# Performance work log

Hardware: AMD Instinct MI355X
Metric: run time of the kernel (lower is better)

The kernel has to match this reference:

```python
import jax, jax.numpy as jnp
import numpy as np

N, F, E, LIN, C, B = 16384, 500, 128, 128, 10, 4096
P_EDGE = 0.002  # ~32 avg degree


def _l2norm(x):
    # F.normalize(dim=1), eps=1e-12
    n = jnp.linalg.norm(x, axis=1, keepdims=True)
    return x / jnp.maximum(n, 1e-12)


def setup_inputs() -> dict:
    key = jax.random.key(0)
    ks = jax.random.split(key, 10)
    adj = (jax.random.uniform(ks[0], (N, N)) < P_EDGE).astype(jnp.float32)
    idx = jnp.arange(N)
    adj = adj.at[idx, idx].set(1.0)  # self-loops guarantee degree >= 1
    data = jax.random.normal(ks[1], (N, F), dtype=jnp.float32)
    nodes = jax.random.randint(ks[2], (B,), 0, N)
    # Encoder 1: Linear(2F -> E); Encoder 2: Linear(2E -> E); classifier heads
    W1 = jax.random.normal(ks[3], (E, 2 * F), dtype=jnp.float32) * 0.03
    b1 = jnp.zeros((E,), jnp.float32)
    W2 = jax.random.normal(ks[4], (E, 2 * E), dtype=jnp.float32) * 0.06
    b2 = jnp.zeros((E,), jnp.float32)
    Wl1 = jax.random.normal(ks[5], (LIN, E), dtype=jnp.float32) * 0.08
    bl1 = jnp.zeros((LIN,), jnp.float32)
    Wl2 = jax.random.normal(ks[6], (C, LIN), dtype=jnp.float32) * 0.12
    bl2 = jnp.zeros((C,), jnp.float32)
    return {"nodes": nodes, "adj": adj, "data": data,
            "W1": W1, "b1": b1, "W2": W2, "b2": b2,
            "Wl1": Wl1, "bl1": bl1, "Wl2": Wl2, "bl2": bl2}


def reference(nodes, adj, data, W1, b1, W2, b2, Wl1, bl1, Wl2, bl2):
    deg = jnp.sum(adj, axis=1, keepdims=True)  # [N,1]
    # Layer 1 (mean aggregator over full neighbor set): computed for all nodes
    neigh1 = (adj @ data) / deg                               # [N,F]
    h1 = jnp.concatenate([data, neigh1], axis=1)              # [N,2F] (self, neigh)
    H1 = _l2norm(jax.nn.relu(h1 @ W1.T + b1))                 # [N,E]
    # Layer 2: only for the queried node batch
    neigh2 = (adj[nodes] @ H1) / deg[nodes]                   # [B,E]
    h2 = jnp.concatenate([H1[nodes], neigh2], axis=1)         # [B,2E]
    H2 = _l2norm(jax.nn.relu(h2 @ W2.T + b2))                 # [B,E]
    x = H2 @ Wl1.T + bl1                                      # [B,LIN]
    x = x @ Wl2.T + bl2                                       # [B,C]
    return jax.nn.softmax(x, axis=1)
```

## Files before the change

### kernel.cpp

```cpp
#include <hip/hip_runtime.h>
#include <math.h>
#include <stddef.h>

#define N_NODES 16384
#define F_DIM   500
#define E_DIM   128
#define C_DIM   10
#define B_DIM   4096
#define MAXDEG  128

typedef __attribute__((ext_vector_type(8))) short short8;
typedef __attribute__((ext_vector_type(4))) float f32x4;

__device__ inline unsigned short f2bf(float f) {
    union { float f; unsigned int u; } v; v.f = f;
    unsigned int u = v.u;
    u += 0x7FFFu + ((u >> 16) & 1u);
    return (unsigned short)(u >> 16);
}
__device__ inline float bf2f(unsigned short u) {
    union { unsigned int u; float f; } v; v.u = (unsigned int)u << 16;
    return v.f;
}
__device__ inline short8 cvt8(float4 a, float4 b) {
    short8 v;
    v[0] = (short)f2bf(a.x); v[1] = (short)f2bf(a.y);
    v[2] = (short)f2bf(a.z); v[3] = (short)f2bf(a.w);
    v[4] = (short)f2bf(b.x); v[5] = (short)f2bf(b.y);
    v[6] = (short)f2bf(b.z); v[7] = (short)f2bf(b.w);
    return v;
}

__global__ __launch_bounds__(256) void k_fuse1(const float* __restrict__ data,
                                               const float* __restrict__ W1,
                                               const float* __restrict__ W2,
                                               const float* __restrict__ Wl1,
                                               const float* __restrict__ adj,
                                               unsigned short* __restrict__ Xb16,
                                               unsigned short* __restrict__ nbr,
                                               int* __restrict__ deg,
                                               unsigned short* __restrict__ W2ab16,
                                               unsigned short* __restrict__ W2bb16,
                                               float* __restrict__ Wl1t) {
    __shared__ alignas(16) unsigned char smem[4352];
    const int bb = blockIdx.x;
    const int tid = threadIdx.x;

    if (bb < 64) {
        int idx = bb * 256 + tid;
        int n = idx >> 7, k = idx & 127;
        W2ab16[idx] = f2bf(W2[(size_t)n * 256 + k]);
        return;
    } else if (bb < 128) {
        int idx = (bb - 64) * 256 + tid;
        int n = idx >> 7, k = idx & 127;
        W2bb16[idx] = f2bf(W2[(size_t)n * 256 + 128 + k]);
        return;
    } else if (bb < 144) {
        float (*tile)[33] = (float (*)[33])smem;
        int tb = bb - 128;
        int k0 = (tb & 3) * 32, e0 = (tb >> 2) * 32;
        int tx = tid & 31, ty0 = tid >> 5;
#pragma unroll
        for (int q = 0; q < 4; ++q) {
            int ty = ty0 + q * 8;
            tile[ty][tx] = Wl1[(size_t)(e0 + ty) * 128 + k0 + tx];
        }
        __syncthreads();
#pragma unroll
        for (int q = 0; q < 4; ++q) {
            int ty = ty0 + q * 8;
            Wl1t[(size_t)(k0 + ty) * 128 + e0 + tx] = tile[tx][ty];
        }
        return;
    } else if (bb < 656) {
        const int g = bb - 144;
        const int blockM = g * 32;
        const int w    = tid >> 6;
        const int lane = tid & 63;
        const int l16  = lane & 15;
        const int quad = lane >> 4;
        f32x4 acc[2][4] = {};
#pragma unroll 2
        for (int c = 0; c < 16; ++c) {
            const int kq = (c << 5) + quad * 8;
            const bool ok0 = (kq + 4 <= F_DIM);
            const bool ok1 = (kq + 8 <= F_DIM);
            short8 af[2], bfr[4];
#pragma unroll
            for (int mt = 0; mt < 2; ++mt) {
                const float* ap = data + (size_t)(blockM + mt * 16 + l16) * F_DIM + kq;
                float4 f0 = ok0 ? *(const float4*)ap       : make_float4(0.f, 0.f, 0.f, 0.f);
                float4 f1 = ok1 ? *(const float4*)(ap + 4) : make_float4(0.f, 0.f, 0.f, 0.f);
                af[mt] = cvt8(f0, f1);
            }
#pragma unroll
            for (int nt = 0; nt < 4; ++nt) {
                int n = w * 64 + nt * 16 + l16;
                const float* bp = W1 + (size_t)(n & 127) * 1000 + (n >> 7) * F_DIM + kq;
                float4 g0 = ok0 ? *(const float4*)bp       : make_float4(0.f, 0.f, 0.f, 0.f);
                float4 g1 = ok1 ? *(const float4*)(bp + 4) : make_float4(0.f, 0.f, 0.f, 0.f);
                bfr[nt] = cvt8(g0, g1);
            }
#pragma unroll
            for (int mt = 0; mt < 2; ++mt)
#pragma unroll
                for (int nt = 0; nt < 4; ++nt)
                    acc[mt][nt] = __builtin_amdgcn_mfma_f32_16x16x32_bf16(af[mt], bfr[nt], acc[mt][nt], 0, 0, 0);
        }
#pragma unroll
        for (int mt = 0; mt < 2; ++mt)
#pragma unroll
            for (int nt = 0; nt < 4; ++nt) {
                int col = w * 64 + nt * 16 + l16;
#pragma unroll
                for (int r = 0; r < 4; ++r) {
                    int row = blockM + mt * 16 + quad * 4 + r;
                    Xb16[(size_t)row * 256 + col] = f2bf(acc[mt][nt][r]);
                }
            }
    } else {
        const int i = bb - 656;
        int* s_cnt = (int*)smem;
        int* s_idx = ((int*)smem) + 4;
        const float4* row4 = (const float4*)(adj + (size_t)i * N_NODES);
        if (tid == 0) *s_cnt = 0;
        __syncthreads();
        float4 v[16];
#pragma unroll
        for (int p = 0; p < 16; ++p) v[p] = row4[p * 256 + tid];
#pragma unroll
        for (int p = 0; p < 16; ++p) {
            int col = p * 1024 + tid * 4;
            if (v[p].x != 0.f) { int q = atomicAdd(s_cnt, 1); if (q < MAXDEG) s_idx[q] = col;     }
            if (v[p].y != 0.f) { int q = atomicAdd(s_cnt, 1); if (q < MAXDEG) s_idx[q] = col + 1; }
            if (v[p].z != 0.f) { int q = atomicAdd(s_cnt, 1); if (q < MAXDEG) s_idx[q] = col + 2; }
            if (v[p].w != 0.f) { int q = atomicAdd(s_cnt, 1); if (q < MAXDEG) s_idx[q] = col + 3; }
        }
        __syncthreads();
        int cnt = *s_cnt; if (cnt > MAXDEG) cnt = MAXDEG;
        if (tid < cnt) nbr[(size_t)i * MAXDEG + tid] = (unsigned short)s_idx[tid];
        if (tid == 0) deg[i] = cnt;
    }
}

__global__ __launch_bounds__(256) void k_gather(const unsigned short* __restrict__ nbr,
                                                const int* __restrict__ deg,
                                                const unsigned short* __restrict__ Xb16,
                                                const float* __restrict__ b1,
                                                unsigned short* __restrict__ H1b) {
    const int lane = threadIdx.x & 63;
    const int i = blockIdx.x * 4 + (threadIdx.x >> 6);
    const int cnt = deg[i];
    const int myn  = (lane < cnt)      ? (int)nbr[(size_t)i * MAXDEG + lane]      : 0;
    const int myn2 = (lane + 64 < cnt) ? (int)nbr[(size_t)i * MAXDEG + lane + 64] : 0;
    const int half = lane >> 5, l32 = lane & 31;
    float ax = 0.f, ay = 0.f, az = 0.f, aw = 0.f;
    for (int k = half; k < cnt; k += 2) {
        int kk = k & 63;
        int j1 = __shfl(myn, kk);
        int j2 = __shfl(myn2, kk);
        int j = (k < 64) ? j1 : j2;
        ushort4 x4 = *(const ushort4*)(Xb16 + (size_t)j * 256 + 128 + l32 * 4);
        ax += bf2f(x4.x); ay += bf2f(x4.y); az += bf2f(x4.z); aw += bf2f(x4.w);
    }
    ax += __shfl_xor(ax, 32); ay += __shfl_xor(ay, 32);
    az += __shfl_xor(az, 32); aw += __shfl_xor(aw, 32);
    ushort4 sx = *(const ushort4*)(Xb16 + (size_t)i * 256 + l32 * 4);
    float4 bb = *(const float4*)(b1 + l32 * 4);
    float fc = (float)cnt;
    float v0 = fmaxf(bf2f(sx.x) + ax / fc + bb.x, 0.f);
    float v1 = fmaxf(bf2f(sx.y) + ay / fc + bb.y, 0.f);
    float v2 = fmaxf(bf2f(sx.z) + az / fc + bb.z, 0.f);
    float v3 = fmaxf(bf2f(sx.w) + aw / fc + bb.w, 0.f);
    float s = v0 * v0 + v1 * v1 + v2 * v2 + v3 * v3;
#pragma unroll
    for (int off = 16; off > 0; off >>= 1) s += __shfl_xor(s, off);
    float rden = 1.0f / fmaxf(sqrtf(s), 1e-12f);
    if (half == 0) {
        ushort4 o;
        o.x = f2bf(v0 * rden); o.y = f2bf(v1 * rden);
        o.z = f2bf(v2 * rden); o.w = f2bf(v3 * rden);
        *(ushort4*)(H1b + (size_t)i * 128 + l32 * 4) = o;
    }
}

__global__ __launch_bounds__(256) void k_gemm2(const unsigned short* __restrict__ H1b,
                                               const unsigned short* __restrict__ W2bb16,
                                               const unsigned short* __restrict__ W2ab16,
                                               const int* __restrict__ nodes,
                                               unsigned short* __restrict__ Yb16,
                                               float* __restrict__ Ya) {
    const int bb = blockIdx.x;
    const bool selfp = (bb >= 512);
    const unsigned short* B = selfp ? W2ab16 : W2bb16;
    const int blockM = (selfp ? (bb - 512) : bb) * 32;
    const int tid  = threadIdx.x;
    const int w    = tid >> 6;
    const int lane = tid & 63;
    const int l16  = lane & 15;
    const int quad = lane >> 4;
    int rsrc0 = blockM + l16,      rsrc1 = blockM + 16 + l16;
    if (selfp) { rsrc0 = nodes[rsrc0]; rsrc1 = nodes[rsrc1]; }
    short8 af[2][4], bfr[2][4];
#pragma unroll
    for (int c = 0; c < 4; ++c) {
        af[0][c] = *(const short8*)(H1b + (size_t)rsrc0 * 128 + c * 32 + quad * 8);
        af[1][c] = *(const short8*)(H1b + (size_t)rsrc1 * 128 + c * 32 + quad * 8);
    }
#pragma unroll
    for (int nt = 0; nt < 2; ++nt) {
        int n = w * 32 + nt * 16 + l16;
#pragma unroll
        for (int c = 0; c < 4; ++c)
            bfr[nt][c] = *(const short8*)(B + (size_t)n * 128 + c * 32 + quad * 8);
    }
    f32x4 acc[2][2] = {};
#pragma unroll
    for (int c = 0; c < 4; ++c)
#pragma unroll
        for (int mt = 0; mt < 2; ++mt)
#pragma unroll
            for (int nt = 0; nt < 2; ++nt)
                acc[mt][nt] = __builtin_amdgcn_mfma_f32_16x16x32_bf16(af[mt][c], bfr[nt][c], acc[mt][nt], 0, 0, 0);
#pragma unroll
    for (int mt = 0; mt < 2; ++mt)
#pragma unroll
        for (int nt = 0; nt < 2; ++nt) {
            int col = w * 32 + nt * 16 + l16;
#pragma unroll
            for (int r = 0; r < 4; ++r) {
                int row = blockM + mt * 16 + quad * 4 + r;
                if (selfp) Ya[(size_t)row * 128 + col] = acc[mt][nt][r];
                else       Yb16[(size_t)row * 128 + col] = f2bf(acc[mt][nt][r]);
            }
        }
}

__global__ __launch_bounds__(256) void k_l2head(const int* __restrict__ nodes,
                                                const unsigned short* __restrict__ nbr,
                                                const int* __restrict__ deg,
                                                const unsigned short* __restrict__ Yb16,
                                                const float* __restrict__ Ya,
                                                const float* __restrict__ b2,
                                                const float* __restrict__ Wl1t,
                                                const float* __restrict__ bl1,
                                                const float* __restrict__ Wl2,
                                                const float* __restrict__ bl2,
                                                float* __restrict__ out) {
    const int lane = threadIdx.x & 63;
    const int b = blockIdx.x * 4 + (threadIdx.x >> 6);
    const int n = nodes[b];
    const int cnt = deg[n];
    const int myn  = (lane < cnt)      ? (int)nbr[(size_t)n * MAXDEG + lane]      : 0;
    const int myn2 = (lane + 64 < cnt) ? (int)nbr[(size_t)n * MAXDEG + lane + 64] : 0;
    const int half = lane >> 5, l32 = lane & 31;
    float ax = 0.f, ay = 0.f, az = 0.f, aw = 0.f;
    for (int k = half; k < cnt; k += 2) {
        int kk = k & 63;
        int j1 = __shfl(myn, kk);
        int j2 = __shfl(myn2, kk);
        int j = (k < 64) ? j1 : j2;
        ushort4 y4 = *(const ushort4*)(Yb16 + (size_t)j * 128 + l32 * 4);
        ax += bf2f(y4.x); ay += bf2f(y4.y); az += bf2f(y4.z); aw += bf2f(y4.w);
    }
    ax += __shfl_xor(ax, 32); ay += __shfl_xor(ay, 32);
    az += __shfl_xor(az, 32); aw += __shfl_xor(aw, 32);
    float4 ya = *(const float4*)(Ya + (size_t)b * 128 + l32 * 4);
    float4 bb = *(const float4*)(b2 + l32 * 4);
    float fc = (float)cnt;
    float h0 = fmaxf(ya.x + ax / fc + bb.x, 0.f);
    float h1 = fmaxf(ya.y + ay / fc + bb.y, 0.f);
    float h2 = fmaxf(ya.z + az / fc + bb.z, 0.f);
    float h3 = fmaxf(ya.w + aw / fc + bb.w, 0.f);
    float s = h0 * h0 + h1 * h1 + h2 * h2 + h3 * h3;
#pragma unroll
    for (int off = 16; off > 0; off >>= 1) s += __shfl_xor(s, off);
    float rden = 1.0f / fmaxf(sqrtf(s), 1e-12f);
    h0 *= rden; h1 *= rden; h2 *= rden; h3 *= rden;
    float2 bl = *(const float2*)(bl1 + 2 * lane);
    float x0 = bl.x, x1 = bl.y;
    const float* wl = Wl1t + 2 * lane;
    for (int m = 0; m < 32; ++m) {
        float k0 = __shfl(h0, m), k1 = __shfl(h1, m), k2 = __shfl(h2, m), k3 = __shfl(h3, m);
        float2 w0 = *(const float2*)(wl + (size_t)(m * 4 + 0) * 128);
        float2 w1 = *(const float2*)(wl + (size_t)(m * 4 + 1) * 128);
        float2 w2 = *(const float2*)(wl + (size_t)(m * 4 + 2) * 128);
        float2 w3 = *(const float2*)(wl + (size_t)(m * 4 + 3) * 128);
        x0 += k0 * w0.x + k1 * w1.x + k2 * w2.x + k3 * w3.x;
        x1 += k0 * w0.y + k1 * w1.y + k2 * w2.y + k3 * w3.y;
    }
    float cv[C_DIM];
#pragma unroll
    for (int cc = 0; cc < C_DIM; ++cc) {
        float2 w = *(const float2*)(Wl2 + (size_t)cc * 128 + 2 * lane);
        float p = x0 * w.x + x1 * w.y;
#pragma unroll
        for (int off = 32; off > 0; off >>= 1) p += __shfl_xor(p, off);
        cv[cc] = p + bl2[cc];
    }
    float mx = cv[0];
#pragma unroll
    for (int cc = 1; cc < C_DIM; ++cc) mx = fmaxf(mx, cv[cc]);
    float se = 0.f;
#pragma unroll
    for (int cc = 0; cc < C_DIM; ++cc) { cv[cc] = expf(cv[cc] - mx); se += cv[cc]; }
    float rse = 1.0f / se;
    float o = cv[0];
#pragma unroll
    for (int cc = 1; cc < C_DIM; ++cc) o = (lane == cc) ? cv[cc] : o;
    if (lane < C_DIM) out[(size_t)b * C_DIM + lane] = o * rse;
}

extern "C" void kernel_launch(void* const* d_in, const int* in_sizes, int n_in,
                              void* d_out, int out_size, void* d_ws, size_t ws_size,
                              hipStream_t stream) {
    const int*   nodes = (const int*)  d_in[0];
    const float* adj   = (const float*)d_in[1];
    const float* data  = (const float*)d_in[2];
    const float* W1    = (const float*)d_in[3];
    const float* b1    = (const float*)d_in[4];
    const float* W2    = (const float*)d_in[5];
    const float* b2    = (const float*)d_in[6];
    const float* Wl1   = (const float*)d_in[7];
    const float* bl1   = (const float*)d_in[8];
    const float* Wl2   = (const float*)d_in[9];
    const float* bl2   = (const float*)d_in[10];
    float* out = (float*)d_out;

    float* Wl1t = (float*)d_ws;
    float* Ya   = Wl1t + 16384;
    unsigned short* W2ab16 = (unsigned short*)(Ya + (size_t)B_DIM * 128);
    unsigned short* W2bb16 = W2ab16 + 16384;
    unsigned short* Xb16   = W2bb16 + 16384;
    unsigned short* H1b    = Xb16 + (size_t)N_NODES * 256;
    unsigned short* Yb16   = H1b + (size_t)N_NODES * 128;
    unsigned short* nbr    = Yb16 + (size_t)N_NODES * 128;
    int* deg = (int*)(nbr + (size_t)N_NODES * MAXDEG);

    k_fuse1<<<144 + 512 + N_NODES, 256, 0, stream>>>(data, W1, W2, Wl1, adj,
                                                     Xb16, nbr, deg,
                                                     W2ab16, W2bb16, Wl1t);
    k_gather<<<N_NODES / 4, 256, 0, stream>>>(nbr, deg, Xb16, b1, H1b);
    k_gemm2<<<512 + 128, 256, 0, stream>>>(H1b, W2bb16, W2ab16, nodes, Yb16, Ya);
    k_l2head<<<B_DIM / 4, 256, 0, stream>>>(nodes, nbr, deg, Yb16, Ya, b2,
                                            Wl1t, bl1, Wl2, bl2, out);
}
```

Before: 1.443 ms.

## Fuse adjacency scan with layer-1 neighbor gather into one per-row kernel

```diff
diff --git a/kernel.cpp b/kernel.cpp
--- a/kernel.cpp
+++ b/kernel.cpp
@@ -31,18 +31,15 @@
     return v;
 }
 
-__global__ __launch_bounds__(256) void k_fuse1(const float* __restrict__ data,
+__global__ __launch_bounds__(256) void k_prep1(const float* __restrict__ data,
                                                const float* __restrict__ W1,
                                                const float* __restrict__ W2,
                                                const float* __restrict__ Wl1,
-                                               const float* __restrict__ adj,
                                                unsigned short* __restrict__ Xb16,
-                                               unsigned short* __restrict__ nbr,
-                                               int* __restrict__ deg,
                                                unsigned short* __restrict__ W2ab16,
                                                unsigned short* __restrict__ W2bb16,
                                                float* __restrict__ Wl1t) {
-    __shared__ alignas(16) unsigned char smem[4352];
+    __shared__ float tile[32][33];
     const int bb = blockIdx.x;
     const int tid = threadIdx.x;
 
@@ -57,7 +54,6 @@
         W2bb16[idx] = f2bf(W2[(size_t)n * 256 + 128 + k]);
         return;
     } else if (bb < 144) {
-        float (*tile)[33] = (float (*)[33])smem;
         int tb = bb - 128;
         int k0 = (tb & 3) * 32, e0 = (tb >> 2) * 32;
         int tx = tid & 31, ty0 = tid >> 5;
@@ -73,115 +69,110 @@
             Wl1t[(size_t)(k0 + ty) * 128 + e0 + tx] = tile[tx][ty];
         }
         return;
-    } else if (bb < 656) {
-        const int g = bb - 144;
-        const int blockM = g * 32;
-        const int w    = tid >> 6;
-        const int lane = tid & 63;
-        const int l16  = lane & 15;
-        const int quad = lane >> 4;
-        f32x4 acc[2][4] = {};
+    }
+    const int g = bb - 144;
+    const int blockM = g * 32;
+    const int w    = tid >> 6;
+    const int lane = tid & 63;
+    const int l16  = lane & 15;
+    const int quad = lane >> 4;
+    f32x4 acc[2][4] = {};
 #pragma unroll 2
-        for (int c = 0; c < 16; ++c) {
-            const int kq = (c << 5) + quad * 8;
-            const bool ok0 = (kq + 4 <= F_DIM);
-            const bool ok1 = (kq + 8 <= F_DIM);
-            short8 af[2], bfr[4];
-#pragma unroll
-            for (int mt = 0; mt < 2; ++mt) {
-                const float* ap = data + (size_t)(blockM + mt * 16 + l16) * F_DIM + kq;
-                float4 f0 = ok0 ? *(const float4*)ap       : make_float4(0.f, 0.f, 0.f, 0.f);
-                float4 f1 = ok1 ? *(const float4*)(ap + 4) : make_float4(0.f, 0.f, 0.f, 0.f);
-                af[mt] = cvt8(f0, f1);
+    for (int c = 0; c < 16; ++c) {
+        const int kq = (c << 5) + quad * 8;
+        const bool ok0 = (kq + 4 <= F_DIM);
+        const bool ok1 = (kq + 8 <= F_DIM);
+        short8 af[2], bfr[4];
+#pragma unroll
+        for (int mt = 0; mt < 2; ++mt) {
+            const float* ap = data + (size_t)(blockM + mt * 16 + l16) * F_DIM + kq;
+            float4 f0 = ok0 ? *(const float4*)ap       : make_float4(0.f, 0.f, 0.f, 0.f);
+            float4 f1 = ok1 ? *(const float4*)(ap + 4) : make_float4(0.f, 0.f, 0.f, 0.f);
+            af[mt] = cvt8(f0, f1);
+        }
+#pragma unroll
+        for (int nt = 0; nt < 4; ++nt) {
+            int n = w * 64 + nt * 16 + l16;
+            const float* bp = W1 + (size_t)(n & 127) * 1000 + (n >> 7) * F_DIM + kq;
+            float4 g0 = ok0 ? *(const float4*)bp       : make_float4(0.f, 0.f, 0.f, 0.f);
+            float4 g1 = ok1 ? *(const float4*)(bp + 4) : make_float4(0.f, 0.f, 0.f, 0.f);
+            bfr[nt] = cvt8(g0, g1);
+        }
+#pragma unroll
+        for (int mt = 0; mt < 2; ++mt)
+#pragma unroll
+            for (int nt = 0; nt < 4; ++nt)
+                acc[mt][nt] = __builtin_amdgcn_mfma_f32_16x16x32_bf16(af[mt], bfr[nt], acc[mt][nt], 0, 0, 0);
+    }
+#pragma unroll
+    for (int mt = 0; mt < 2; ++mt)
+#pragma unroll
+        for (int nt = 0; nt < 4; ++nt) {
+            int col = w * 64 + nt * 16 + l16;
+#pragma unroll
+            for (int r = 0; r < 4; ++r) {
+                int row = blockM + mt * 16 + quad * 4 + r;
+                Xb16[(size_t)row * 256 + col] = f2bf(acc[mt][nt][r]);
             }
-#pragma unroll
-            for (int nt = 0; nt < 4; ++nt) {
-                int n = w * 64 + nt * 16 + l16;
-                const float* bp = W1 + (size_t)(n & 127) * 1000 + (n >> 7) * F_DIM + kq;
-                float4 g0 = ok0 ? *(const float4*)bp       : make_float4(0.f, 0.f, 0.f, 0.f);
-                float4 g1 = ok1 ? *(const float4*)(bp + 4) : make_float4(0.f, 0.f, 0.f, 0.f);
-                bfr[nt] = cvt8(g0, g1);
-            }
-#pragma unroll
-            for (int mt = 0; mt < 2; ++mt)
-#pragma unroll
-                for (int nt = 0; nt < 4; ++nt)
-                    acc[mt][nt] = __builtin_amdgcn_mfma_f32_16x16x32_bf16(af[mt], bfr[nt], acc[mt][nt], 0, 0, 0);
-        }
-#pragma unroll
-        for (int mt = 0; mt < 2; ++mt)
-#pragma unroll
-            for (int nt = 0; nt < 4; ++nt) {
-                int col = w * 64 + nt * 16 + l16;
-#pragma unroll
-                for (int r = 0; r < 4; ++r) {
-                    int row = blockM + mt * 16 + quad * 4 + r;
-                    Xb16[(size_t)row * 256 + col] = f2bf(acc[mt][nt][r]);
-                }
-            }
-    } else {
-        const int i = bb - 656;
-        int* s_cnt = (int*)smem;
-        int* s_idx = ((int*)smem) + 4;
-        const float4* row4 = (const float4*)(adj + (size_t)i * N_NODES);
-        if (tid == 0) *s_cnt = 0;
-        __syncthreads();
-        float4 v[16];
-#pragma unroll
-        for (int p = 0; p < 16; ++p) v[p] = row4[p * 256 + tid];
-#pragma unroll
-        for (int p = 0; p < 16; ++p) {
-            int col = p * 1024 + tid * 4;
-            if (v[p].x != 0.f) { int q = atomicAdd(s_cnt, 1); if (q < MAXDEG) s_idx[q] = col;     }
-            if (v[p].y != 0.f) { int q = atomicAdd(s_cnt, 1); if (q < MAXDEG) s_idx[q] = col + 1; }
-            if (v[p].z != 0.f) { int q = atomicAdd(s_cnt, 1); if (q < MAXDEG) s_idx[q] = col + 2; }
-            if (v[p].w != 0.f) { int q = atomicAdd(s_cnt, 1); if (q < MAXDEG) s_idx[q] = col + 3; }
-        }
-        __syncthreads();
-        int cnt = *s_cnt; if (cnt > MAXDEG) cnt = MAXDEG;
-        if (tid < cnt) nbr[(size_t)i * MAXDEG + tid] = (unsigned short)s_idx[tid];
-        if (tid == 0) deg[i] = cnt;
-    }
-}
-
-__global__ __launch_bounds__(256) void k_gather(const unsigned short* __restrict__ nbr,
-                                                const int* __restrict__ deg,
-                                                const unsigned short* __restrict__ Xb16,
-                                                const float* __restrict__ b1,
-                                                unsigned short* __restrict__ H1b) {
-    const int lane = threadIdx.x & 63;
-    const int i = blockIdx.x * 4 + (threadIdx.x >> 6);
-    const int cnt = deg[i];
-    const int myn  = (lane < cnt)      ? (int)nbr[(size_t)i * MAXDEG + lane]      : 0;
-    const int myn2 = (lane + 64 < cnt) ? (int)nbr[(size_t)i * MAXDEG + lane + 64] : 0;
-    const int half = lane >> 5, l32 = lane & 31;
-    float ax = 0.f, ay = 0.f, az = 0.f, aw = 0.f;
-    for (int k = half; k < cnt; k += 2) {
-        int kk = k & 63;
-        int j1 = __shfl(myn, kk);
-        int j2 = __shfl(myn2, kk);
-        int j = (k < 64) ? j1 : j2;
-        ushort4 x4 = *(const ushort4*)(Xb16 + (size_t)j * 256 + 128 + l32 * 4);
-        ax += bf2f(x4.x); ay += bf2f(x4.y); az += bf2f(x4.z); aw += bf2f(x4.w);
-    }
-    ax += __shfl_xor(ax, 32); ay += __shfl_xor(ay, 32);
-    az += __shfl_xor(az, 32); aw += __shfl_xor(aw, 32);
-    ushort4 sx = *(const ushort4*)(Xb16 + (size_t)i * 256 + l32 * 4);
-    float4 bb = *(const float4*)(b1 + l32 * 4);
-    float fc = (float)cnt;
-    float v0 = fmaxf(bf2f(sx.x) + ax / fc + bb.x, 0.f);
-    float v1 = fmaxf(bf2f(sx.y) + ay / fc + bb.y, 0.f);
-    float v2 = fmaxf(bf2f(sx.z) + az / fc + bb.z, 0.f);
-    float v3 = fmaxf(bf2f(sx.w) + aw / fc + bb.w, 0.f);
-    float s = v0 * v0 + v1 * v1 + v2 * v2 + v3 * v3;
-#pragma unroll
-    for (int off = 16; off > 0; off >>= 1) s += __shfl_xor(s, off);
-    float rden = 1.0f / fmaxf(sqrtf(s), 1e-12f);
-    if (half == 0) {
-        ushort4 o;
-        o.x = f2bf(v0 * rden); o.y = f2bf(v1 * rden);
-        o.z = f2bf(v2 * rden); o.w = f2bf(v3 * rden);
-        *(ushort4*)(H1b + (size_t)i * 128 + l32 * 4) = o;
+        }
+}
+
+__global__ __launch_bounds__(256) void k_scan_gather(const float* __restrict__ adj,
+                                                     const unsigned short* __restrict__ Xb16,
+                                                     const float* __restrict__ b1,
+                                                     unsigned short* __restrict__ nbr,
+                                                     int* __restrict__ deg,
+                                                     unsigned short* __restrict__ H1b) {
+    const int i = blockIdx.x;
+    const int tid = threadIdx.x;
+    __shared__ int s_cnt;
+    __shared__ int s_idx[MAXDEG];
+    __shared__ float s_part[8][128];
+    __shared__ float s_w[2];
+
+    const float4* row4 = (const float4*)(adj + (size_t)i * N_NODES);
+    if (tid == 0) s_cnt = 0;
+    __syncthreads();
+    float4 v[16];
+#pragma unroll
+    for (int p = 0; p < 16; ++p) v[p] = row4[p * 256 + tid];
+#pragma unroll
+    for (int p = 0; p < 16; ++p) {
+        int col = p * 1024 + tid * 4;
+        if (v[p].x != 0.f) { int q = atomicAdd(&s_cnt, 1); if (q < MAXDEG) s_idx[q] = col;     }
+        if (v[p].y != 0.f) { int q = atomicAdd(&s_cnt, 1); if (q < MAXDEG) s_idx[q] = col + 1; }
+        if (v[p].z != 0.f) { int q = atomicAdd(&s_cnt, 1); if (q < MAXDEG) s_idx[q] = col + 2; }
+        if (v[p].w != 0.f) { int q = atomicAdd(&s_cnt, 1); if (q < MAXDEG) s_idx[q] = col + 3; }
+    }
+    __syncthreads();
+    int cnt = s_cnt; if (cnt > MAXDEG) cnt = MAXDEG;
+    if (tid < cnt) nbr[(size_t)i * MAXDEG + tid] = (unsigned short)s_idx[tid];
+    if (tid == 0) deg[i] = cnt;
+
+    const int g = tid >> 5, l = tid & 31;
+    float4 a4 = make_float4(0.f, 0.f, 0.f, 0.f);
+    for (int k = g; k < cnt; k += 8) {
+        ushort4 x4 = ((const ushort4*)(Xb16 + (size_t)s_idx[k] * 256 + 128))[l];
+        a4.x += bf2f(x4.x); a4.y += bf2f(x4.y); a4.z += bf2f(x4.z); a4.w += bf2f(x4.w);
+    }
+    *(float4*)&s_part[g][l * 4] = a4;
+    __syncthreads();
+    float vv = 0.f;
+    if (tid < 128) {
+        float tot = 0.f;
+#pragma unroll
+        for (int g2 = 0; g2 < 8; ++g2) tot += s_part[g2][tid];
+        vv = bf2f(Xb16[(size_t)i * 256 + tid]) + tot / (float)cnt + b1[tid];
+        vv = fmaxf(vv, 0.f);
+        float s = vv * vv;
+#pragma unroll
+        for (int off = 32; off > 0; off >>= 1) s += __shfl_down(s, off, 64);
+        if ((tid & 63) == 0) s_w[tid >> 6] = s;
+    }
+    __syncthreads();
+    if (tid < 128) {
+        float denom = fmaxf(sqrtf(s_w[0] + s_w[1]), 1e-12f);
+        H1b[(size_t)i * 128 + tid] = f2bf(vv / denom);
     }
 }
 
@@ -338,10 +329,9 @@
     unsigned short* nbr    = Yb16 + (size_t)N_NODES * 128;
     int* deg = (int*)(nbr + (size_t)N_NODES * MAXDEG);
 
-    k_fuse1<<<144 + 512 + N_NODES, 256, 0, stream>>>(data, W1, W2, Wl1, adj,
-                                                     Xb16, nbr, deg,
-                                                     W2ab16, W2bb16, Wl1t);
-    k_gather<<<N_NODES / 4, 256, 0, stream>>>(nbr, deg, Xb16, b1, H1b);
+    k_prep1<<<656, 256, 0, stream>>>(data, W1, W2, Wl1,
+                                     Xb16, W2ab16, W2bb16, Wl1t);
+    k_scan_gather<<<N_NODES, 256, 0, stream>>>(adj, Xb16, b1, nbr, deg, H1b);
     k_gemm2<<<512 + 128, 256, 0, stream>>>(H1b, W2bb16, W2ab16, nodes, Yb16, Ya);
     k_l2head<<<B_DIM / 4, 256, 0, stream>>>(nodes, nbr, deg, Yb16, Ya, b2,
                                             Wl1t, bl1, Wl2, bl2, out);
```

New measurement: 1.434 ms. About the same (-0.7%).
